# Optimization experiments

Hardware: AMD Instinct MI355X
Metric: run time of the kernel (lower is better)

## Reference

```python
import jax, jax.numpy as jnp
import numpy as np

B, T, K = 512, 1024, 48
START, STOP, PAD = 45, 46, 47
NEG = -10000.0


def setup_inputs() -> dict:
    key = jax.random.key(0)
    k1, k2, k3 = jax.random.split(key, 3)
    h_tag = jax.random.normal(k1, (B, T, K), dtype=jnp.float32)
    # valid lengths in [T//2, T]; mask is float (used multiplicatively in the blend)
    lengths = jax.random.randint(k2, (B,), T // 2, T + 1)
    mask = (jnp.arange(T)[None, :] < lengths[:, None]).astype(jnp.float32)
    trans = jax.random.normal(k3, (K, K), dtype=jnp.float32)
    # replicate the CRF constraint initialization from the torch module
    trans = (trans.at[START, :].set(NEG)
                  .at[:, STOP].set(NEG)
                  .at[:, PAD].set(NEG)
                  .at[PAD, :].set(NEG)
                  .at[PAD, STOP].set(0.0)
                  .at[PAD, PAD].set(0.0))
    return {"h_tag": h_tag, "mask": mask, "trans": trans}


def _lse(x):
    # matches the module's log_sum_exp over the last axis
    m = jnp.max(x, axis=-1)
    return m + jnp.log(jnp.sum(jnp.exp(x - m[..., None]), axis=-1))


def reference(h_tag, mask, trans):
    Bsz, Tlen, Ktags = h_tag.shape
    score0 = jnp.full((Bsz, Ktags), NEG, dtype=h_tag.dtype).at[:, STOP].set(0.0)

    def step(score, xs):
        emit_t, mask_t = xs  # emit_t: [B, K], mask_t: [B]
        # score[b, j] + trans[i, j] + emit_t[b, i] -> [B, K(next=i), K(prev=j)]
        s = score[:, None, :] + trans[None, :, :] + emit_t[:, :, None]
        s = _lse(s)  # [B, K]
        m = mask_t[:, None]
        return s * m + score * (1.0 - m), None

    xs = (jnp.swapaxes(h_tag, 0, 1), mask.T)  # time-major for scan
    score, _ = jax.lax.scan(step, score0, xs)
    return _lse(score + trans[STOP])  # [B] log partition scores
```

## Files before the change

### kernel.cpp

```cpp
#include <hip/hip_runtime.h>
#include <hip/hip_bf16.h>

#define Bsz   512
#define Tlen  1024
#define Ktag  48
#define NREAL 45
#define HALF_T 512
#define STOPT 46
#define NEGV  -10000.0f

__device__ __forceinline__ float wave_max(float v) {
#pragma unroll
    for (int off = 32; off > 0; off >>= 1)
        v = fmaxf(v, __shfl_xor(v, off, 64));
    return v;
}

__device__ __forceinline__ float wave_sum(float v) {
#pragma unroll
    for (int off = 32; off > 0; off >>= 1)
        v += __shfl_xor(v, off, 64);
    return v;
}

__device__ __forceinline__ float bcast(float v, int l) {
    return __int_as_float(__builtin_amdgcn_readlane(__float_as_int(v), l));
}

template <bool BF16>
__device__ __forceinline__ float ld(const void* p, size_t i) {
    if constexpr (BF16) {
        unsigned int u = ((const unsigned short*)p)[i];
        return __uint_as_float(u << 16);
    } else {
        return ((const float*)p)[i];
    }
}

template <bool BF16>
__device__ void crf_chains(const void* __restrict__ h, const void* __restrict__ mask,
                           const void* __restrict__ trans, float* __restrict__ ws) {
    __shared__ float ltr[Ktag][Ktag + 1];
    const int lane = threadIdx.x;
    const int bid  = blockIdx.x;
    const bool fwd = bid < Bsz;
    const int b    = fwd ? bid : bid - Bsz;

    for (int idx = lane; idx < Ktag * Ktag; idx += 64) {
        int i = idx / Ktag;
        ltr[i][idx - i * Ktag] = ld<BF16>(trans, (size_t)idx);
    }
    __syncthreads();

    float E[Ktag];
#pragma unroll
    for (int j = 0; j < Ktag; j++) E[j] = 0.f;
    if (lane < Ktag) {
        if (fwd) {
#pragma unroll
            for (int j = 0; j < Ktag; j++) E[j] = __expf(ltr[lane][j]);
        } else {
#pragma unroll
            for (int i = 0; i < Ktag; i++) E[i] = __expf(ltr[i][lane]);
        }
    }

    const int li = (lane < Ktag) ? lane : (Ktag - 1);
    const size_t hb = (size_t)b * Tlen * Ktag;

    float* uF = ws;
    float* MF = ws + (size_t)Bsz * Ktag;
    float* uB = MF + Bsz;
    float* MB = uB + (size_t)Bsz * Ktag;

    float u = 0.f, M = 0.f;

    if (fwd) {
        {
            float e0 = ld<BF16>(h, hb + li);
            float mx = -3.0e38f;
#pragma unroll
            for (int j = 0; j < Ktag; j++) {
                float v = ltr[li][j] + (j == STOPT ? 0.f : NEGV);
                mx = fmaxf(mx, v);
            }
            float s = 0.f;
#pragma unroll
            for (int j = 0; j < Ktag; j++) {
                float v = ltr[li][j] + (j == STOPT ? 0.f : NEGV);
                s += __expf(v - mx);
            }
            float sc = e0 + mx + __logf(s);
            if (lane >= NREAL) sc = -3.0e38f;
            float m1 = wave_max(sc);
            M = m1;
            u = (lane < NREAL) ? __expf(sc - m1) : 0.f;
        }
        float em[4], emn[4];
#pragma unroll
        for (int k = 0; k < 4; k++) {
            int tt = 1 + k; if (tt > HALF_T - 1) tt = HALF_T - 1;
            em[k] = ld<BF16>(h, hb + (size_t)tt * Ktag + li);
        }
        for (int t = 1; t < HALF_T; t += 4) {
#pragma unroll
            for (int k = 0; k < 4; k++) {
                int tt = t + 4 + k; if (tt > HALF_T - 1) tt = HALF_T - 1;
                emn[k] = ld<BF16>(h, hb + (size_t)tt * Ktag + li);
            }
#pragma unroll
            for (int k = 0; k < 4; k++) {
                if (t + k < HALF_T) {
                    float ee = __expf(em[k]);
                    float a0 = 0.f, a1 = 0.f, a2 = 0.f, a3 = 0.f;
#pragma unroll
                    for (int j = 0; j < Ktag; j += 4) {
                        a0 = fmaf(E[j + 0], bcast(u, j + 0), a0);
                        a1 = fmaf(E[j + 1], bcast(u, j + 1), a1);
                        a2 = fmaf(E[j + 2], bcast(u, j + 2), a2);
                        a3 = fmaf(E[j + 3], bcast(u, j + 3), a3);
                    }
                    u = ((a0 + a1) + (a2 + a3)) * ee;
                }
            }
            float m = wave_max(u);
            u *= 1.0f / m;
            M += __logf(m);
#pragma unroll
            for (int k = 0; k < 4; k++) em[k] = emn[k];
        }
        if (lane < Ktag) uF[(size_t)b * Ktag + lane] = u;
        if (lane == 0) MF[b] = M;
    } else {
        float c = 0.f;
        for (int t0 = lane; t0 < Tlen; t0 += 64)
            c += ld<BF16>(mask, (size_t)b * Tlen + t0);
        c = wave_sum(c);
        int len = (int)(c + 0.5f);

        float g = (lane < Ktag) ? ltr[STOPT][lane] : -3.0e38f;
        float m0 = wave_max(g);
        M = m0;
        u = (lane < Ktag) ? __expf(g - m0) : 0.f;

        int t0 = len - 1;
        float em[4], emn[4];
#pragma unroll
        for (int k = 0; k < 4; k++) {
            int tt = t0 - k; if (tt < HALF_T) tt = HALF_T;
            em[k] = ld<BF16>(h, hb + (size_t)tt * Ktag + li);
        }
        for (int tg = t0; tg >= HALF_T; tg -= 4) {
#pragma unroll
            for (int k = 0; k < 4; k++) {
                int tt = tg - 4 - k; if (tt < HALF_T) tt = HALF_T;
                emn[k] = ld<BF16>(h, hb + (size_t)tt * Ktag + li);
            }
#pragma unroll
            for (int k = 0; k < 4; k++) {
                if (tg - k >= HALF_T) {
                    float ee = __expf(em[k]);
                    float v = u * ee;
                    float a0 = 0.f, a1 = 0.f, a2 = 0.f, a3 = 0.f;
#pragma unroll
                    for (int j = 0; j < Ktag; j += 4) {
                        a0 = fmaf(E[j + 0], bcast(v, j + 0), a0);
                        a1 = fmaf(E[j + 1], bcast(v, j + 1), a1);
                        a2 = fmaf(E[j + 2], bcast(v, j + 2), a2);
                        a3 = fmaf(E[j + 3], bcast(v, j + 3), a3);
                    }
                    u = (a0 + a1) + (a2 + a3);
                }
            }
            float m = wave_max(u);
            u *= 1.0f / m;
            M += __logf(m);
#pragma unroll
            for (int k = 0; k < 4; k++) em[k] = emn[k];
        }
        if (lane < Ktag) uB[(size_t)b * Ktag + lane] = u;
        if (lane == 0) MB[b] = M;
    }
}

__global__ void __launch_bounds__(64) crf_main(const void* __restrict__ h,
                                               const void* __restrict__ mask,
                                               const void* __restrict__ trans,
                                               float* __restrict__ ws) {
    bool isbf16 = (((const unsigned short*)mask)[0] == 0x3F80);
    if (isbf16) crf_chains<true>(h, mask, trans, ws);
    else        crf_chains<false>(h, mask, trans, ws);
}

__global__ void __launch_bounds__(64) crf_combine(const void* __restrict__ mask,
                                                  const float* __restrict__ ws,
                                                  void* __restrict__ out) {
    const int b = blockIdx.x;
    const int lane = threadIdx.x;
    const float* uF = ws;
    const float* MF = ws + (size_t)Bsz * Ktag;
    const float* uB = MF + Bsz;
    const float* MB = uB + (size_t)Bsz * Ktag;

    float p = (lane < Ktag) ? uF[(size_t)b * Ktag + lane] * uB[(size_t)b * Ktag + lane] : 0.f;
    float s = wave_sum(p);
    float ans = MF[b] + MB[b] + __logf(s);

    bool isbf16 = (((const unsigned short*)mask)[0] == 0x3F80);
    if (lane == 0) {
        if (isbf16) {
            unsigned int x = __float_as_uint(ans);
            unsigned int r = (x + 0x7FFFu + ((x >> 16) & 1u)) >> 16;
            ((unsigned short*)out)[b] = (unsigned short)r;
        } else {
            ((float*)out)[b] = ans;
        }
    }
}

extern "C" void kernel_launch(void* const* d_in, const int* in_sizes, int n_in,
                              void* d_out, int out_size, void* d_ws, size_t ws_size,
                              hipStream_t stream) {
    const void* h     = d_in[0];
    const void* mask  = d_in[1];
    const void* trans = d_in[2];
    float* ws = (float*)d_ws;

    hipLaunchKernelGGL(crf_main, dim3(2 * Bsz), dim3(64), 0, stream, h, mask, trans, ws);
    hipLaunchKernelGGL(crf_combine, dim3(Bsz), dim3(64), 0, stream, mask, ws, d_out);
}
```

Before: 247.4 us.

## Batch 16 sequences per wave and run CRF recurrence on bf16 MFMA

Moves the per-step 48x48 matrix-vector recurrence onto 16x16x16 bf16 MFMA instructions, with each wave handling 16 batch rows at once, so only 64 waves do work instead of 1024. The transition matrix is split into bf16 high and low parts to recover precision, and a runtime probe works out the MFMA operand layout before choosing this path, falling back to the VALU kernel otherwise. The backward chain now runs a fixed 512 steps with masking instead of starting at each sequence's length. Risks are lower occupancy (only 64 active waves on a large GPU), the per-step latency of a serial chain of MFMAs, and precision loss from rounding the state vector to bf16.

```diff
diff --git a/kernel.cpp b/kernel.cpp
--- a/kernel.cpp
+++ b/kernel.cpp
@@ -8,6 +8,21 @@
 #define HALF_T 512
 #define STOPT 46
 #define NEGV  -10000.0f
+#define GB    16
+
+typedef float          f32x4  __attribute__((ext_vector_type(4)));
+typedef short          bf16x4 __attribute__((ext_vector_type(4)));
+typedef unsigned short u16x4  __attribute__((ext_vector_type(4)));
+
+#if defined(__has_builtin)
+#  if __has_builtin(__builtin_amdgcn_mfma_f32_16x16x16bf16_1k)
+#    define HAVE_MFMA16 1
+#  endif
+#endif
+#ifndef HAVE_MFMA16
+#  define HAVE_MFMA16 0
+#endif
+
 
 __device__ __forceinline__ float wave_max(float v) {
 #pragma unroll
@@ -15,14 +30,12 @@
         v = fmaxf(v, __shfl_xor(v, off, 64));
     return v;
 }
-
 __device__ __forceinline__ float wave_sum(float v) {
 #pragma unroll
     for (int off = 32; off > 0; off >>= 1)
         v += __shfl_xor(v, off, 64);
     return v;
 }
-
 __device__ __forceinline__ float bcast(float v, int l) {
     return __int_as_float(__builtin_amdgcn_readlane(__float_as_int(v), l));
 }
@@ -37,10 +50,347 @@
     }
 }
 
+__device__ __forceinline__ unsigned pk2(float lo, float hi) {
+    unsigned r;
+    asm("v_cvt_pk_bf16_f32 %0, %1, %2" : "=v"(r) : "v"(lo), "v"(hi));
+    return r;
+}
+__device__ __forceinline__ bf16x4 mk4(unsigned a, unsigned b) {
+    union { unsigned u[2]; bf16x4 v; } c; c.u[0] = a; c.u[1] = b; return c.v;
+}
+
+template <bool BF16> struct EmT { using T = f32x4; };
+template <>          struct EmT<true> { using T = u16x4; };
+
+__device__ __forceinline__ f32x4 tof4(f32x4 v) { return v; }
+__device__ __forceinline__ f32x4 tof4(u16x4 v) {
+    f32x4 r;
+    r.x = __uint_as_float((unsigned)v.x << 16);
+    r.y = __uint_as_float((unsigned)v.y << 16);
+    r.z = __uint_as_float((unsigned)v.z << 16);
+    r.w = __uint_as_float((unsigned)v.w << 16);
+    return r;
+}
+
+#if HAVE_MFMA16
+__device__ __forceinline__ f32x4 mfma16(bf16x4 a, bf16x4 b, f32x4 c) {
+    return __builtin_amdgcn_mfma_f32_16x16x16bf16_1k(a, b, c, 0, 0, 0);
+}
+
+__device__ __forceinline__ bf16x4 pk4(f32x4 u) {
+    return mk4(pk2(u.x, u.y), pk2(u.z, u.w));
+}
+__device__ __forceinline__ bf16x4 pkmul(f32x4 u, f32x4 e) {
+    return mk4(pk2(u.x * __expf(e.x), u.y * __expf(e.y)),
+               pk2(u.z * __expf(e.z), u.w * __expf(e.w)));
+}
+__device__ __forceinline__ f32x4 mulexp(f32x4 a, f32x4 e) {
+    f32x4 r;
+    r.x = a.x * __expf(e.x); r.y = a.y * __expf(e.y);
+    r.z = a.z * __expf(e.z); r.w = a.w * __expf(e.w);
+    return r;
+}
+__device__ __forceinline__ f32x4 sel4(bool a, f32x4 x, f32x4 y) {
+    f32x4 r;
+    r.x = a ? x.x : y.x; r.y = a ? x.y : y.y;
+    r.z = a ? x.z : y.z; r.w = a ? x.w : y.w;
+    return r;
+}
+
+__device__ __forceinline__ int Ft1(int i, int k) { return ((3*i + 5*k) % 7) - 3; }
+__device__ __forceinline__ int Gt1(int k, int c) { return ((2*k + 3*c) % 5) - 2; }
+__device__ __forceinline__ int Ft2(int i, int k) { return ((5*i + 7*k) % 11) - 5; }
+__device__ __forceinline__ int Gt2(int k, int c) { return ((3*k + 2*c) % 9) - 4; }
+
+__device__ int probe_layout() {
+    const int lane = threadIdx.x & 63;
+    const int b = lane & 15, g = lane >> 4;
+    float e1[4], e2[4];
+#pragma unroll
+    for (int r = 0; r < 4; r++) {
+        int s1 = 0, s2 = 0;
+        for (int k = 0; k < 16; k++) {
+            s1 += Ft1(4*g + r, k) * Gt1(k, b);
+            s2 += Ft2(4*g + r, k) * Gt2(k, b);
+        }
+        e1[r] = (float)s1; e2[r] = (float)s2;
+    }
+    int found = -1;
+    for (int av = 0; av < 3; av++) {
+        for (int bv = 0; bv < 3; bv++) {
+            float A1[4], B1[4], A2[4], B2[4];
+#pragma unroll
+            for (int j = 0; j < 4; j++) {
+                int ar, ak, bk, bc;
+                if (av == 0)      { ar = b;       ak = 4*g + j; }
+                else if (av == 1) { ar = b;       ak = g + 4*j; }
+                else              { ar = 4*g + j; ak = b;       }
+                if (bv == 0)      { bk = 4*g + j; bc = b;       }
+                else if (bv == 1) { bk = g + 4*j; bc = b;       }
+                else              { bk = b;       bc = 4*g + j; }
+                A1[j] = (float)Ft1(ar, ak);  B1[j] = (float)Gt1(bk, bc);
+                A2[j] = (float)Ft2(ar, ak);  B2[j] = (float)Gt2(bk, bc);
+            }
+            f32x4 z = {0.f, 0.f, 0.f, 0.f};
+            f32x4 d1 = mfma16(mk4(pk2(A1[0],A1[1]), pk2(A1[2],A1[3])),
+                              mk4(pk2(B1[0],B1[1]), pk2(B1[2],B1[3])), z);
+            f32x4 d2 = mfma16(mk4(pk2(A2[0],A2[1]), pk2(A2[2],A2[3])),
+                              mk4(pk2(B2[0],B2[1]), pk2(B2[2],B2[3])), z);
+            bool ok = d1.x==e1[0] && d1.y==e1[1] && d1.z==e1[2] && d1.w==e1[3]
+                   && d2.x==e2[0] && d2.y==e2[1] && d2.z==e2[2] && d2.w==e2[3];
+            if (__all(ok) && found < 0) found = av*3 + bv;
+        }
+    }
+    return found;
+}
+
 template <bool BF16>
-__device__ void crf_chains(const void* __restrict__ h, const void* __restrict__ mask,
-                           const void* __restrict__ trans, float* __restrict__ ws) {
-    __shared__ float ltr[Ktag][Ktag + 1];
+__device__ void crf_mfma(const void* __restrict__ h, const void* __restrict__ mask,
+                         const void* __restrict__ trans, float* __restrict__ ws,
+                         int amap, float (*ltr)[Ktag + 1], float* lse) {
+    using ET = typename EmT<BF16>::T;
+    constexpr size_t esz = BF16 ? 2 : 4;
+
+    const int lane = threadIdx.x;
+    const int gw   = blockIdx.x;
+    const bool fwd = gw < (Bsz / GB);
+    const int b0   = (fwd ? gw : gw - (Bsz / GB)) * GB;
+    const int b    = lane & 15;
+    const int g    = lane >> 4;
+
+    for (int idx = lane; idx < Ktag * Ktag; idx += 64)
+        ltr[idx / Ktag][idx % Ktag] = ld<BF16>(trans, (size_t)idx);
+    __syncthreads();
+
+    if (fwd && lane < Ktag) {
+        float mx = -3.0e38f;
+        for (int j = 0; j < Ktag; j++)
+            mx = fmaxf(mx, ltr[lane][j] + (j == STOPT ? 0.f : NEGV));
+        float s = 0.f;
+        for (int j = 0; j < Ktag; j++)
+            s += __expf(ltr[lane][j] + (j == STOPT ? 0.f : NEGV) - mx);
+        lse[lane] = mx + __logf(s);
+    }
+    __syncthreads();
+
+    bf16x4 Eh[3][3], El[3][3];
+#pragma unroll
+    for (int m = 0; m < 3; m++) {
+#pragma unroll
+        for (int c = 0; c < 3; c++) {
+            float x[4];
+#pragma unroll
+            for (int j = 0; j < 4; j++) {
+                int rr, kk;
+                if (amap == 0)      { rr = b;       kk = 4*g + j; }
+                else if (amap == 1) { rr = b;       kk = g + 4*j; }
+                else                { rr = 4*g + j; kk = b;       }
+                int R = 16*m + rr, K = 16*c + kk;
+                x[j] = fwd ? __expf(ltr[R][K]) : __expf(ltr[K][R]);
+            }
+            unsigned h01 = pk2(x[0], x[1]), h23 = pk2(x[2], x[3]);
+            Eh[m][c] = mk4(h01, h23);
+            float l0 = x[0] - __uint_as_float(h01 << 16);
+            float l1 = x[1] - __uint_as_float(h01 & 0xFFFF0000u);
+            float l2 = x[2] - __uint_as_float(h23 << 16);
+            float l3 = x[3] - __uint_as_float(h23 & 0xFFFF0000u);
+            El[m][c] = mk4(pk2(l0, l1), pk2(l2, l3));
+        }
+    }
+
+    const char* hb = (const char*)h + ((size_t)(b0 + b) * Tlen * Ktag + 4 * g) * esz;
+
+    float* uF = ws;
+    float* MF = ws + (size_t)Bsz * Ktag;
+    float* uB = MF + Bsz;
+    float* MB = uB + (size_t)Bsz * Ktag;
+
+    f32x4 U[3];
+    float M;
+    int lenv = 0;
+
+    if (fwd) {
+        f32x4 e0[3];
+#pragma unroll
+        for (int c = 0; c < 3; c++)
+            e0[c] = tof4(*(const ET*)(hb + (size_t)(16 * c) * esz));
+        float cmax = -3.0e38f;
+        float sc[3][4];
+#pragma unroll
+        for (int c = 0; c < 3; c++)
+#pragma unroll
+            for (int j = 0; j < 4; j++) {
+                int i = 16*c + 4*g + j;
+                float v = (i < NREAL) ? (e0[c][j] + lse[i]) : -3.0e38f;
+                sc[c][j] = v;
+                cmax = fmaxf(cmax, v);
+            }
+        cmax = fmaxf(cmax, __shfl_xor(cmax, 16, 64));
+        cmax = fmaxf(cmax, __shfl_xor(cmax, 32, 64));
+        M = cmax;
+#pragma unroll
+        for (int c = 0; c < 3; c++)
+#pragma unroll
+            for (int j = 0; j < 4; j++)
+                U[c][j] = (16*c + 4*g + j < NREAL) ? __expf(sc[c][j] - cmax) : 0.f;
+    } else {
+        const char* mb = (const char*)mask + (size_t)(b0 + b) * Tlen * esz;
+        float cs = 0.f;
+        for (int kk = 0; kk < Tlen / 16; kk++) {
+            f32x4 v = tof4(*(const ET*)(mb + (size_t)(kk * 16 + 4 * g) * esz));
+            cs += (v.x + v.y) + (v.z + v.w);
+        }
+        cs += __shfl_xor(cs, 16, 64);
+        cs += __shfl_xor(cs, 32, 64);
+        lenv = (int)(cs + 0.5f);
+
+        float cmax = -3.0e38f;
+        float gv[3][4];
+#pragma unroll
+        for (int c = 0; c < 3; c++)
+#pragma unroll
+            for (int j = 0; j < 4; j++) {
+                gv[c][j] = ltr[STOPT][16*c + 4*g + j];
+                cmax = fmaxf(cmax, gv[c][j]);
+            }
+        cmax = fmaxf(cmax, __shfl_xor(cmax, 16, 64));
+        cmax = fmaxf(cmax, __shfl_xor(cmax, 32, 64));
+        M = cmax;
+#pragma unroll
+        for (int c = 0; c < 3; c++)
+#pragma unroll
+            for (int j = 0; j < 4; j++)
+                U[c][j] = __expf(gv[c][j] - cmax);
+    }
+
+    if (fwd) {
+        ET em[4][3], emn[4][3];
+#pragma unroll
+        for (int k = 0; k < 4; k++)
+#pragma unroll
+            for (int c = 0; c < 3; c++)
+                em[k][c] = *(const ET*)(hb + ((size_t)(1 + k) * Ktag + 16*c) * esz);
+        for (int t = 1; t < HALF_T; t += 4) {
+#pragma unroll
+            for (int k = 0; k < 4; k++) {
+                int tt = t + 4 + k; if (tt > HALF_T - 1) tt = HALF_T - 1;
+#pragma unroll
+                for (int c = 0; c < 3; c++)
+                    emn[k][c] = *(const ET*)(hb + ((size_t)tt * Ktag + 16*c) * esz);
+            }
+#pragma unroll
+            for (int k = 0; k < 4; k++) {
+                if (t + k < HALF_T) {
+                    bf16x4 V[3];
+#pragma unroll
+                    for (int c = 0; c < 3; c++) V[c] = pk4(U[c]);
+                    f32x4 a0 = {0.f,0.f,0.f,0.f};
+                    f32x4 a1 = {0.f,0.f,0.f,0.f};
+                    f32x4 a2 = {0.f,0.f,0.f,0.f};
+#pragma unroll
+                    for (int c = 0; c < 3; c++) {
+                        a0 = mfma16(Eh[0][c], V[c], a0);
+                        a1 = mfma16(Eh[1][c], V[c], a1);
+                        a2 = mfma16(Eh[2][c], V[c], a2);
+                    }
+#pragma unroll
+                    for (int c = 0; c < 3; c++) {
+                        a0 = mfma16(El[0][c], V[c], a0);
+                        a1 = mfma16(El[1][c], V[c], a1);
+                        a2 = mfma16(El[2][c], V[c], a2);
+                    }
+                    U[0] = mulexp(a0, tof4(em[k][0]));
+                    U[1] = mulexp(a1, tof4(em[k][1]));
+                    U[2] = mulexp(a2, tof4(em[k][2]));
+                }
+            }
+            float mx = fmaxf(fmaxf(U[0].x, U[0].y), fmaxf(U[0].z, U[0].w));
+            mx = fmaxf(mx, fmaxf(fmaxf(U[1].x, U[1].y), fmaxf(U[1].z, U[1].w)));
+            mx = fmaxf(mx, fmaxf(fmaxf(U[2].x, U[2].y), fmaxf(U[2].z, U[2].w)));
+            mx = fmaxf(mx, __shfl_xor(mx, 16, 64));
+            mx = fmaxf(mx, __shfl_xor(mx, 32, 64));
+            float inv = 1.0f / mx;
+            U[0] *= inv; U[1] *= inv; U[2] *= inv;
+            M += __logf(mx);
+#pragma unroll
+            for (int k = 0; k < 4; k++)
+#pragma unroll
+                for (int c = 0; c < 3; c++) em[k][c] = emn[k][c];
+        }
+#pragma unroll
+        for (int c = 0; c < 3; c++)
+#pragma unroll
+            for (int j = 0; j < 4; j++)
+                uF[(size_t)(b0 + b) * Ktag + 16*c + 4*g + j] = U[c][j];
+        if (lane < GB) MF[b0 + lane] = M;
+    } else {
+        ET em[4][3], emn[4][3];
+#pragma unroll
+        for (int k = 0; k < 4; k++)
+#pragma unroll
+            for (int c = 0; c < 3; c++)
+                em[k][c] = *(const ET*)(hb + ((size_t)(Tlen - 1 - k) * Ktag + 16*c) * esz);
+        for (int tg = Tlen - 1; tg >= HALF_T; tg -= 4) {
+#pragma unroll
+            for (int k = 0; k < 4; k++) {
+                int tt = tg - 4 - k; if (tt < HALF_T) tt = HALF_T;
+#pragma unroll
+                for (int c = 0; c < 3; c++)
+                    emn[k][c] = *(const ET*)(hb + ((size_t)tt * Ktag + 16*c) * esz);
+            }
+#pragma unroll
+            for (int k = 0; k < 4; k++) {
+                const int t = tg - k;
+                const bool act = (t < lenv);
+                bf16x4 V[3];
+#pragma unroll
+                for (int c = 0; c < 3; c++) V[c] = pkmul(U[c], tof4(em[k][c]));
+                f32x4 a0 = {0.f,0.f,0.f,0.f};
+                f32x4 a1 = {0.f,0.f,0.f,0.f};
+                f32x4 a2 = {0.f,0.f,0.f,0.f};
+#pragma unroll
+                for (int c = 0; c < 3; c++) {
+                    a0 = mfma16(Eh[0][c], V[c], a0);
+                    a1 = mfma16(Eh[1][c], V[c], a1);
+                    a2 = mfma16(Eh[2][c], V[c], a2);
+                }
+#pragma unroll
+                for (int c = 0; c < 3; c++) {
+                    a0 = mfma16(El[0][c], V[c], a0);
+                    a1 = mfma16(El[1][c], V[c], a1);
+                    a2 = mfma16(El[2][c], V[c], a2);
+                }
+                U[0] = sel4(act, a0, U[0]);
+                U[1] = sel4(act, a1, U[1]);
+                U[2] = sel4(act, a2, U[2]);
+            }
+            float mx = fmaxf(fmaxf(U[0].x, U[0].y), fmaxf(U[0].z, U[0].w));
+            mx = fmaxf(mx, fmaxf(fmaxf(U[1].x, U[1].y), fmaxf(U[1].z, U[1].w)));
+            mx = fmaxf(mx, fmaxf(fmaxf(U[2].x, U[2].y), fmaxf(U[2].z, U[2].w)));
+            mx = fmaxf(mx, __shfl_xor(mx, 16, 64));
+            mx = fmaxf(mx, __shfl_xor(mx, 32, 64));
+            float inv = 1.0f / mx;
+            U[0] *= inv; U[1] *= inv; U[2] *= inv;
+            M += __logf(mx);
+#pragma unroll
+            for (int k = 0; k < 4; k++)
+#pragma unroll
+                for (int c = 0; c < 3; c++) em[k][c] = emn[k][c];
+        }
+#pragma unroll
+        for (int c = 0; c < 3; c++)
+#pragma unroll
+            for (int j = 0; j < 4; j++)
+                uB[(size_t)(b0 + b) * Ktag + 16*c + 4*g + j] = U[c][j];
+        if (lane < GB) MB[b0 + lane] = M;
+    }
+}
+#endif
+
+template <bool BF16>
+__device__ void crf_valu(const void* __restrict__ h, const void* __restrict__ mask,
+                         const void* __restrict__ trans, float* __restrict__ ws,
+                         float (*ltr)[Ktag + 1]) {
     const int lane = threadIdx.x;
     const int bid  = blockIdx.x;
     const bool fwd = bid < Bsz;
@@ -187,9 +537,23 @@
                                                const void* __restrict__ mask,
                                                const void* __restrict__ trans,
                                                float* __restrict__ ws) {
+    __shared__ float ltr_s[Ktag][Ktag + 1];
+#if HAVE_MFMA16
+    __shared__ float lse_s[Ktag];
+#endif
     bool isbf16 = (((const unsigned short*)mask)[0] == 0x3F80);
-    if (isbf16) crf_chains<true>(h, mask, trans, ws);
-    else        crf_chains<false>(h, mask, trans, ws);
+#if HAVE_MFMA16
+    int lay = probe_layout();
+    if (lay >= 0 && (lay % 3) == 0) {
+        if (blockIdx.x >= (2 * Bsz) / GB) return;
+        int amap = lay / 3;
+        if (isbf16) crf_mfma<true >(h, mask, trans, ws, amap, ltr_s, lse_s);
+        else        crf_mfma<false>(h, mask, trans, ws, amap, ltr_s, lse_s);
+        return;
+    }
+#endif
+    if (isbf16) crf_valu<true >(h, mask, trans, ws, ltr_s);
+    else        crf_valu<false>(h, mask, trans, ws, ltr_s);
 }
 
 __global__ void __launch_bounds__(64) crf_combine(const void* __restrict__ mask,
```

Result: slower. 262.2 us (+6.0%).
